# Kernel tuning notes

Hardware: AMD Instinct MI355X
Metric: run time of the kernel (lower is better)

## Reference

```python
import jax, jax.numpy as jnp
import numpy as np

D = 128          # hidden_dim
H = 4            # num attention heads (torch default nhead=4 in this module)
DH = D // H
NA = 4096        # author nodes
NP = 100000      # paper nodes
EAP = 500000     # author->paper edges
EPA = 500000     # paper->author edges
DFF = 2048       # TransformerEncoderLayer FFN dim (torch default)
OUT = 16
IN_A = 128
IN_P = 256
EPS = 1e-5


def layer_norm(x, g, b):
    mu = jnp.mean(x, -1, keepdims=True)
    var = jnp.mean((x - mu) ** 2, -1, keepdims=True)
    return (x - mu) / jnp.sqrt(var + EPS) * g + b


def scatter_mean(vals, idx, n):
    # torch_scatter 'mean': empty segments yield 0
    s = jax.ops.segment_sum(vals, idx, num_segments=n)
    c = jax.ops.segment_sum(jnp.ones((vals.shape[0], 1), vals.dtype), idx, num_segments=n)
    return s / jnp.maximum(c, 1.0)


def metapath_layer(x_src, x_dst, src, dst, Wv, bv, Wo, bo, g, b):
    # nn.MultiheadAttention applied per-edge with seq_len=1 (query/key/value are
    # [1, E, D]); softmax over a single key is identically 1, so the attention
    # output is exactly out_proj(v_proj(x_src[src])) -- q/k projections have no
    # effect on the output (and zero gradient).
    v = x_src[src] @ Wv.T + bv            # [E, D] gather + value projection
    attn = v @ Wo.T + bo                  # output projection
    agg = scatter_mean(attn, dst, x_dst.shape[0])
    return layer_norm(agg + x_dst, g, b)


def fusion_layer(x, Wqkv, bqkv, Wo, bo, W1, b1, W2, b2, g1, bt1, g2, bt2):
    # torch TransformerEncoderLayer defaults: post-norm, relu, batch_first=False,
    # so x: [S=NA (seq), M (batch = #metapaths), D].
    S, M, _ = x.shape
    qkv = x @ Wqkv.T + bqkv               # [S, M, 3D]
    q, k, v = jnp.split(qkv, 3, axis=-1)
    q = q.reshape(S, M, H, DH)
    k = k.reshape(S, M, H, DH)
    v = v.reshape(S, M, H, DH)
    scores = jnp.einsum('smhd,tmhd->mhst', q, k) / np.float32(np.sqrt(DH))
    a = jax.nn.softmax(scores, axis=-1)
    ctx = jnp.einsum('mhst,tmhd->smhd', a, v).reshape(S, M, D)
    x = layer_norm(x + ctx @ Wo.T + bo, g1, bt1)
    ff = jax.nn.relu(x @ W1.T + b1) @ W2.T + b2
    return layer_norm(x + ff, g2, bt2)


def setup_inputs() -> dict:
    key = jax.random.key(0)
    ks = iter(jax.random.split(key, 64))
    def nrm(shape, scale=0.02):
        return jax.random.normal(next(ks), shape, dtype=jnp.float32) * scale
    inp = {
        'x_author': jax.random.normal(next(ks), (NA, IN_A), dtype=jnp.float32),
        'x_paper': jax.random.normal(next(ks), (NP, IN_P), dtype=jnp.float32),
        'src_ap': jax.random.randint(next(ks), (EAP,), 0, NA),
        'dst_ap': jax.random.randint(next(ks), (EAP,), 0, NP),
        'src_pa': jax.random.randint(next(ks), (EPA,), 0, NP),
        'dst_pa': jax.random.randint(next(ks), (EPA,), 0, NA),
        'pa_W': nrm((D, IN_A)), 'pa_b': nrm((D,)),
        'pp_W': nrm((D, IN_P)), 'pp_b': nrm((D,)),
        'f_Wqkv': nrm((3 * D, D)), 'f_bqkv': nrm((3 * D,)),
        'f_Wo': nrm((D, D)), 'f_bo': nrm((D,)),
        'f_W1': nrm((DFF, D)), 'f_b1': nrm((DFF,)),
        'f_W2': nrm((D, DFF)), 'f_b2': nrm((D,)),
        'f_g1': jnp.ones((D,), jnp.float32), 'f_bt1': jnp.zeros((D,), jnp.float32),
        'f_g2': jnp.ones((D,), jnp.float32), 'f_bt2': jnp.zeros((D,), jnp.float32),
        'cls_W': nrm((OUT, D)), 'cls_b': nrm((OUT,)),
    }
    for i in range(3):
        inp[f'l{i}_Wv'] = nrm((D, D)); inp[f'l{i}_bv'] = nrm((D,))
        inp[f'l{i}_Wo'] = nrm((D, D)); inp[f'l{i}_bo'] = nrm((D,))
        inp[f'l{i}_g'] = jnp.ones((D,), jnp.float32); inp[f'l{i}_b'] = jnp.zeros((D,), jnp.float32)
    return inp


def reference(x_author, x_paper, src_ap, dst_ap, src_pa, dst_pa,
              pa_W, pa_b, pp_W, pp_b,
              f_Wqkv, f_bqkv, f_Wo, f_bo, f_W1, f_b1, f_W2, f_b2,
              f_g1, f_bt1, f_g2, f_bt2, cls_W, cls_b,
              l0_Wv, l0_bv, l0_Wo, l0_bo, l0_g, l0_b,
              l1_Wv, l1_bv, l1_Wo, l1_bo, l1_g, l1_b,
              l2_Wv, l2_bv, l2_Wo, l2_bo, l2_g, l2_b):
    # project node features to hidden_dim
    ha = x_author @ pa_W.T + pa_b         # [NA, D]
    hp = x_paper @ pp_W.T + pp_b          # [NP, D]
    # metapath 0: paper -> author (one MetapathLayer)
    mp0 = metapath_layer(hp, ha, src_pa, dst_pa, l0_Wv, l0_bv, l0_Wo, l0_bo, l0_g, l0_b)
    # metapath 1: author -> paper -> author (two MetapathLayers)
    t = metapath_layer(ha, hp, src_ap, dst_ap, l1_Wv, l1_bv, l1_Wo, l1_bo, l1_g, l1_b)
    mp1 = metapath_layer(t, ha, src_pa, dst_pa, l2_Wv, l2_bv, l2_Wo, l2_bo, l2_g, l2_b)
    stacked = jnp.stack([mp0, mp1], axis=1)   # [NA, 2, D]
    fused = fusion_layer(stacked, f_Wqkv, f_bqkv, f_Wo, f_bo,
                         f_W1, f_b1, f_W2, f_b2,
                         f_g1, f_bt1, f_g2, f_bt2).mean(axis=1)
    return fused @ cls_W.T + cls_b            # [NA, OUT]
```

## Files before the change

### kernel.cpp

```cpp
#include <hip/hip_runtime.h>
#include <math.h>

constexpr int NA = 4096, NP = 100000, E_AP = 500000, E_PA = 500000;
constexpr int D = 128, DFF = 2048, NOUT = 16, IN_A = 128, IN_P = 256;

typedef __attribute__((ext_vector_type(8))) short bf16x8;
typedef __attribute__((ext_vector_type(4))) float f32x4;
typedef unsigned int u32;

__device__ __forceinline__ ushort f2b(float x) {
    union { float f; unsigned u; } v; v.f = x;
    unsigned r = v.u + 0x7fff + ((v.u >> 16) & 1);
    return (ushort)(r >> 16);
}
__device__ __forceinline__ float b2f(ushort h) {
    union { unsigned u; float f; } v; v.u = (unsigned)h << 16;
    return v.f;
}
__device__ __forceinline__ u32 fbits(float x) {
    union { float f; u32 u; } v; v.f = x; return v.u;
}

__device__ __forceinline__ bf16x8 cvtfrag(float4 a, float4 b) {
    union { u32 w[4]; bf16x8 v; } r;
    asm("v_cvt_pk_bf16_f32 %0, %1, %2" : "=v"(r.w[0]) : "v"(a.x), "v"(a.y));
    asm("v_cvt_pk_bf16_f32 %0, %1, %2" : "=v"(r.w[1]) : "v"(a.z), "v"(a.w));
    asm("v_cvt_pk_bf16_f32 %0, %1, %2" : "=v"(r.w[2]) : "v"(b.x), "v"(b.y));
    asm("v_cvt_pk_bf16_f32 %0, %1, %2" : "=v"(r.w[3]) : "v"(b.z), "v"(b.w));
    return r.v;
}

#define GLL(gp, lp) __builtin_amdgcn_global_load_lds( \
    (const __attribute__((address_space(1))) u32*)(gp), \
    (__attribute__((address_space(3))) u32*)(lp), 16, 0, 0)

__global__ __launch_bounds__(256) void gemm_bf16(
    const ushort* __restrict__ Abf, const float* __restrict__ Af32, int lda,
    const ushort* __restrict__ B, int ldb,
    const float* __restrict__ bias,
    float* __restrict__ outf, ushort* __restrict__ outh, int ldc,
    int M, int N, int K, int act)
{
    __shared__ uint8_t lds[(16 + 32) * 1040];
    uint8_t* sAb = lds;
    uint8_t* sBb = lds + 16 * 1040;

    const int wave = threadIdx.x >> 6;
    const int lane = threadIdx.x & 63;
    const int l16 = lane & 15, quad = lane >> 4;
    const int row0 = blockIdx.y * 64;
    const int col0 = blockIdx.x * 128;
    const int wrg = (wave >> 1) * 2;
    const int wc0 = (wave & 1) * 64;
    const int nz = gridDim.z;
    const int ksub = K / nz;
    const int kbeg = blockIdx.z * ksub;
    const int kgrps = ksub >> 7;

    f32x4 acc[2][4] = {};

    const int sr = lane & 15, sc = lane >> 4;
    const int arow = min(row0 + lane, M - 1);
    const int ag = lane >> 4;
    uint8_t* adst = sAb + (ag * 4 + wave) * 1040 + sr * 16;

    for (int grp = 0; grp < kgrps; ++grp) {
        const int kg = kbeg + grp * 128;
        if (grp) __syncthreads();
        #pragma unroll
        for (int gg = 0; gg < 2; ++gg) {
            int g = wave * 2 + gg;
            const ushort* bp = B + (long)(col0 + g * 16 + sr) * ldb + kg + sc * 8;
            #pragma unroll
            for (int s = 0; s < 4; ++s)
                GLL(bp + s * 32, sBb + (g * 4 + s) * 1040);
        }
        if (Af32) {
            const float* ap = Af32 + (long)arow * lda + kg + wave * 32;
            #pragma unroll
            for (int q = 0; q < 4; ++q) {
                float4 f0 = *(const float4*)(ap + q * 8);
                float4 f1 = *(const float4*)(ap + q * 8 + 4);
                *(bf16x8*)(adst + q * 256) = cvtfrag(f0, f1);
            }
        } else {
            const ushort* ap = Abf + (long)arow * lda + kg + wave * 32;
            #pragma unroll
            for (int q = 0; q < 4; ++q)
                *(bf16x8*)(adst + q * 256) = *(const bf16x8*)(ap + q * 8);
        }
        __syncthreads();
        #pragma unroll
        for (int s = 0; s < 4; ++s) {
            bf16x8 af[2], bfr[4];
            #pragma unroll
            for (int i = 0; i < 2; ++i)
                af[i] = *(const bf16x8*)(sAb + ((wrg + i) * 4 + s) * 1040 + lane * 16);
            #pragma unroll
            for (int j = 0; j < 4; ++j)
                bfr[j] = *(const bf16x8*)(sBb + (((wc0 >> 4) + j) * 4 + s) * 1040 + lane * 16);
            #pragma unroll
            for (int i = 0; i < 2; ++i)
                #pragma unroll
                for (int j = 0; j < 4; ++j)
                    acc[i][j] = __builtin_amdgcn_mfma_f32_16x16x32_bf16(
                        af[i], bfr[j], acc[i][j], 0, 0, 0);
        }
    }

    #pragma unroll
    for (int i = 0; i < 2; ++i) {
        #pragma unroll
        for (int r = 0; r < 4; ++r) {
            int row = row0 + wrg * 16 + i * 16 + quad * 4 + r;
            if (row >= M) continue;
            #pragma unroll
            for (int j = 0; j < 4; ++j) {
                int col = col0 + wc0 + j * 16 + l16;
                if (nz > 1) {
                    atomicAdd(&outf[(long)row * ldc + col], acc[i][j][r]);
                } else {
                    float v = acc[i][j][r] + (bias ? bias[col] : 0.f);
                    if (act) v = fmaxf(v, 0.f);
                    if (outf) outf[(long)row * ldc + col] = v;
                    if (outh) outh[(long)row * ldc + col] = f2b(v);
                }
            }
        }
    }
}

__global__ __launch_bounds__(256) void fuse_weights(
    const float* __restrict__ Wv0, const float* __restrict__ bv0,
    const float* __restrict__ Wo0, const float* __restrict__ bo0,
    const float* __restrict__ Wv1, const float* __restrict__ bv1,
    const float* __restrict__ Wo1, const float* __restrict__ bo1,
    const float* __restrict__ Wv2, const float* __restrict__ bv2,
    const float* __restrict__ Wo2, const float* __restrict__ bo2,
    ushort* __restrict__ Wfb, float* __restrict__ beff)
{
    int blk = blockIdx.x;
    if (blk >= 192) {
        int l = blk - 192;
        const float* bv = l == 0 ? bv0 : (l == 1 ? bv1 : bv2);
        const float* Wo = l == 0 ? Wo0 : (l == 1 ? Wo1 : Wo2);
        const float* bo = l == 0 ? bo0 : (l == 1 ? bo1 : bo2);
        if (threadIdx.x < 128) {
            int r = threadIdx.x;
            float acc = bo[r];
            #pragma unroll 8
            for (int j = 0; j < 128; ++j) acc += Wo[r * 128 + j] * bv[j];
            beff[l * 128 + r] = acc;
        }
        return;
    }
    int l = blk >> 6;
    const float* Wv = l == 0 ? Wv0 : (l == 1 ? Wv1 : Wv2);
    const float* Wo = l == 0 ? Wo0 : (l == 1 ? Wo1 : Wo2);
    int r = (blk & 63) * 2 + (threadIdx.x >> 7);
    int c = threadIdx.x & 127;
    float acc = 0.f;
    #pragma unroll 8
    for (int j = 0; j < 128; ++j)
        acc += Wo[r * 128 + j] * Wv[j * 128 + c];
    Wfb[l * 16384 + r * 128 + c] = f2b(acc);
}

__global__ void hist_kernel(const int* __restrict__ dst, int* __restrict__ cnt, int E)
{
    int e = blockIdx.x * 256 + threadIdx.x;
    if (e < E) atomicAdd(&cnt[dst[e]], 1);
}

__global__ __launch_bounds__(256) void scan_local(
    const int* __restrict__ in, int* __restrict__ out,
    int* __restrict__ bsum, int n)
{
    __shared__ int wsum[4];
    int t = threadIdx.x;
    int base = blockIdx.x * 1024 + t * 4;
    int v0 = (base + 0 < n) ? in[base + 0] : 0;
    int v1 = (base + 1 < n) ? in[base + 1] : 0;
    int v2 = (base + 2 < n) ? in[base + 2] : 0;
    int v3 = (base + 3 < n) ? in[base + 3] : 0;
    int tsum = v0 + v1 + v2 + v3;
    int lane = t & 63;
    int x = tsum;
    #pragma unroll
    for (int o = 1; o < 64; o <<= 1) {
        int y = __shfl_up(x, o, 64);
        if (lane >= o) x += y;
    }
    int wid = t >> 6;
    if (lane == 63) wsum[wid] = x;
    __syncthreads();
    int woff = 0;
    #pragma unroll
    for (int ww = 0; ww < 3; ++ww) if (ww < wid) woff += wsum[ww];
    int excl = x - tsum + woff;
    if (base + 0 < n) out[base + 0] = excl;
    if (base + 1 < n) out[base + 1] = excl + v0;
    if (base + 2 < n) out[base + 2] = excl + v0 + v1;
    if (base + 3 < n) out[base + 3] = excl + v0 + v1 + v2;
    if (bsum && t == 255) bsum[blockIdx.x] = excl + tsum;
}

__global__ void scan_add(int* __restrict__ off, const int* __restrict__ bofs, int n)
{
    int i = blockIdx.x * 256 + threadIdx.x;
    if (i < n) off[i] += bofs[i >> 10];
}

__global__ void copy_int_kernel(const int* __restrict__ a, int* __restrict__ b, int n)
{
    int i = blockIdx.x * 256 + threadIdx.x;
    if (i < n) b[i] = a[i];
}

__global__ void fill_csr_kernel(const int* __restrict__ src, const int* __restrict__ dst,
                                int* __restrict__ cur, int* __restrict__ esrc, int E)
{
    int e = blockIdx.x * 256 + threadIdx.x;
    if (e >= E) return;
    int slot = atomicAdd(&cur[dst[e]], 1);
    esrc[slot] = src[e];
}

__global__ __launch_bounds__(256) void gather_mean(
    const ushort* __restrict__ z, const int* __restrict__ off,
    const int* __restrict__ cnt, const int* __restrict__ esrc,
    ushort* __restrict__ outh, int R)
{
    int grp = threadIdx.x >> 5;
    int tg  = threadIdx.x & 31;
    int row = blockIdx.x * 8 + grp;
    if (row >= R) return;
    int e0 = off[row], deg = cnt[row];
    int eend = e0 + deg;
    float a0 = 0.f, a1 = 0.f, a2 = 0.f, a3 = 0.f;
    int e = e0;
    for (; e + 4 <= eend; e += 4) {
        int s0 = esrc[e], s1 = esrc[e + 1], s2 = esrc[e + 2], s3 = esrc[e + 3];
        ushort4 v0 = ((const ushort4*)(z + (long)s0 * 128))[tg];
        ushort4 v1 = ((const ushort4*)(z + (long)s1 * 128))[tg];
        ushort4 v2 = ((const ushort4*)(z + (long)s2 * 128))[tg];
        ushort4 v3 = ((const ushort4*)(z + (long)s3 * 128))[tg];
        a0 += b2f(v0.x) + b2f(v1.x) + b2f(v2.x) + b2f(v3.x);
        a1 += b2f(v0.y) + b2f(v1.y) + b2f(v2.y) + b2f(v3.y);
        a2 += b2f(v0.z) + b2f(v1.z) + b2f(v2.z) + b2f(v3.z);
        a3 += b2f(v0.w) + b2f(v1.w) + b2f(v2.w) + b2f(v3.w);
    }
    for (; e < eend; ++e) {
        int s = esrc[e];
        ushort4 v = ((const ushort4*)(z + (long)s * 128))[tg];
        a0 += b2f(v.x); a1 += b2f(v.y); a2 += b2f(v.z); a3 += b2f(v.w);
    }
    float inv = 1.f / fmaxf((float)deg, 1.f);
    ushort4 h4 = {f2b(a0 * inv), f2b(a1 * inv), f2b(a2 * inv), f2b(a3 * inv)};
    ((ushort4*)(outh + (long)row * 128))[tg] = h4;
}

__global__ __launch_bounds__(256) void gather_mean_ln(
    const ushort* __restrict__ z, const int* __restrict__ off,
    const int* __restrict__ cnt, const int* __restrict__ esrc,
    const ushort* __restrict__ base, const float* __restrict__ g,
    const float* __restrict__ b, ushort* __restrict__ outh, int R)
{
    int grp = threadIdx.x >> 5;
    int tg  = threadIdx.x & 31;
    int row = blockIdx.x * 8 + grp;
    if (row >= R) return;
    int e0 = off[row], deg = cnt[row];
    int eend = e0 + deg;
    float a0 = 0.f, a1 = 0.f, a2 = 0.f, a3 = 0.f;
    int e = e0;
    for (; e + 4 <= eend; e += 4) {
        int s0 = esrc[e], s1 = esrc[e + 1], s2 = esrc[e + 2], s3 = esrc[e + 3];
        ushort4 v0 = ((const ushort4*)(z + (long)s0 * 128))[tg];
        ushort4 v1 = ((const ushort4*)(z + (long)s1 * 128))[tg];
        ushort4 v2 = ((const ushort4*)(z + (long)s2 * 128))[tg];
        ushort4 v3 = ((const ushort4*)(z + (long)s3 * 128))[tg];
        a0 += b2f(v0.x) + b2f(v1.x) + b2f(v2.x) + b2f(v3.x);
        a1 += b2f(v0.y) + b2f(v1.y) + b2f(v2.y) + b2f(v3.y);
        a2 += b2f(v0.z) + b2f(v1.z) + b2f(v2.z) + b2f(v3.z);
        a3 += b2f(v0.w) + b2f(v1.w) + b2f(v2.w) + b2f(v3.w);
    }
    for (; e < eend; ++e) {
        int s = esrc[e];
        ushort4 v = ((const ushort4*)(z + (long)s * 128))[tg];
        a0 += b2f(v.x); a1 += b2f(v.y); a2 += b2f(v.z); a3 += b2f(v.w);
    }
    float inv = 1.f / fmaxf((float)deg, 1.f);
    ushort4 bs = ((const ushort4*)(base + (long)row * 128))[tg];
    float x0 = a0 * inv + b2f(bs.x), x1 = a1 * inv + b2f(bs.y);
    float x2 = a2 * inv + b2f(bs.z), x3 = a3 * inv + b2f(bs.w);
    float s1 = x0 + x1 + x2 + x3;
    #pragma unroll
    for (int o = 1; o < 32; o <<= 1) s1 += __shfl_xor(s1, o, 64);
    float mu = s1 * (1.f / 128.f);
    float d0 = x0 - mu, d1 = x1 - mu, d2 = x2 - mu, d3 = x3 - mu;
    float s2 = d0 * d0 + d1 * d1 + d2 * d2 + d3 * d3;
    #pragma unroll
    for (int o = 1; o < 32; o <<= 1) s2 += __shfl_xor(s2, o, 64);
    float rstd = rsqrtf(s2 * (1.f / 128.f) + 1e-5f);
    float4 gv = ((const float4*)g)[tg];
    float4 bv = ((const float4*)b)[tg];
    ushort4 h4;
    h4.x = f2b(d0 * rstd * gv.x + bv.x);
    h4.y = f2b(d1 * rstd * gv.y + bv.y);
    h4.z = f2b(d2 * rstd * gv.z + bv.z);
    h4.w = f2b(d3 * rstd * gv.w + bv.w);
    ((ushort4*)(outh + (long)row * 128))[tg] = h4;
}

__global__ __launch_bounds__(128) void mean_add_ln(
    const float* __restrict__ a, const float* __restrict__ bias,
    const float* __restrict__ basef, const ushort* __restrict__ baseh,
    const float* __restrict__ g, const float* __restrict__ b,
    float* __restrict__ outf, ushort* __restrict__ outh, int out_ld, int R)
{
    int row = blockIdx.x;
    if (row >= R) return;
    int d = threadIdx.x;
    float x = a[(long)row * 128 + d];
    if (bias) x += bias[d];
    if (basef) x += basef[(long)row * 128 + d];
    if (baseh) x += b2f(baseh[(long)row * 128 + d]);

    __shared__ float red[4];
    float s = x;
    #pragma unroll
    for (int o = 32; o >= 1; o >>= 1) s += __shfl_xor(s, o, 64);
    if ((d & 63) == 0) red[d >> 6] = s;
    __syncthreads();
    float mu = (red[0] + red[1]) * (1.f / 128.f);
    float dx = x - mu;
    float s2 = dx * dx;
    #pragma unroll
    for (int o = 32; o >= 1; o >>= 1) s2 += __shfl_xor(s2, o, 64);
    if ((d & 63) == 0) red[2 + (d >> 6)] = s2;
    __syncthreads();
    float var = (red[2] + red[3]) * (1.f / 128.f);
    float v = dx * rsqrtf(var + 1e-5f) * g[d] + b[d];
    if (outf) outf[(long)row * out_ld + d] = v;
    if (outh) outh[(long)row * out_ld + d] = f2b(v);
}

struct CvtArgs { const float* in[6]; ushort* out[6]; int n4[6]; };
__global__ void cvt_multi(CvtArgs a)
{
    int j = blockIdx.y;
    int i = blockIdx.x * 256 + threadIdx.x;
    if (i >= a.n4[j]) return;
    float4 v = ((const float4*)a.in[j])[i];
    ushort4 o;
    o.x = f2b(v.x); o.y = f2b(v.y); o.z = f2b(v.z); o.w = f2b(v.w);
    ((ushort4*)a.out[j])[i] = o;
}

__global__ __launch_bounds__(256) void flash_attn(
    const ushort* __restrict__ qkvb,
    float* __restrict__ opart, float* __restrict__ lpart_g)
{
    const int qt = blockIdx.x;
    const int mh = blockIdx.y;
    const int ks = blockIdx.z;
    const int m = mh >> 2, h = mh & 3;
    const int wave = threadIdx.x >> 6;
    const int lane = threadIdx.x & 63;
    const int l16 = lane & 15, quad = lane >> 4;

    __shared__ ushort sK[2][64 * 40];
    __shared__ u32    sV[2][32 * 32];
    __shared__ u32    sP[4][16 * 32];

    const int q0 = qt * 64 + wave * 16;
    const float qs = 0.17677669529663687f * 1.4426950408889634f;
    bf16x8 qf;
    {
        bf16x8 qraw = *(const bf16x8*)(qkvb + ((long)(q0 + l16) * 2 + m) * 384 + h * 32 + quad * 8);
        #pragma unroll
        for (int j = 0; j < 8; ++j)
            qf[j] = (short)f2b(b2f((ushort)qraw[j]) * qs);
    }

    f32x4 oacc0 = {0.f, 0.f, 0.f, 0.f};
    f32x4 oacc1 = {0.f, 0.f, 0.f, 0.f};
    float lp = 0.f;

    const int skey = threadIdx.x >> 2, sseg = threadIdx.x & 3;
    const int vkp  = threadIdx.x & 31, vdc  = (threadIdx.x >> 5) * 4;
    const int kbeg = ks * (NA / 4);
    const ushort* kbase = qkvb + ((long)((kbeg + skey) * 2 + m)) * 384 + 128 + h * 32 + sseg * 8;
    const ushort* vbase = qkvb + ((long)((kbeg + vkp * 2) * 2 + m)) * 384 + 256 + h * 32 + vdc;
    const int kwo = skey * 40 + sseg * 8;
    int vwo[4];
    #pragma unroll
    for (int i = 0; i < 4; ++i)
        vwo[i] = (vdc + i) * 32 + ((((vkp >> 2) ^ ((vdc + i) & 7)) << 2) | (vkp & 3));

    bf16x8 kreg = *(const bf16x8*)(kbase);
    ushort4 v0r = *(const ushort4*)(vbase);
    ushort4 v1r = *(const ushort4*)(vbase + 768);
    *(bf16x8*)(&sK[0][kwo]) = kreg;
    sV[0][vwo[0]] = (u32)v0r.x | ((u32)v1r.x << 16);
    sV[0][vwo[1]] = (u32)v0r.y | ((u32)v1r.y << 16);
    sV[0][vwo[2]] = (u32)v0r.z | ((u32)v1r.z << 16);
    sV[0][vwo[3]] = (u32)v0r.w | ((u32)v1r.w << 16);
    __syncthreads();

    int cur = 0;
    for (int kt = 0; kt < 16; ++kt) {
        const bool more = (kt + 1) < 16;
        if (more) {
            long off = (long)(kt + 1) * 64 * 768;
            kreg = *(const bf16x8*)(kbase + off);
            v0r  = *(const ushort4*)(vbase + off);
            v1r  = *(const ushort4*)(vbase + off + 768);
        }

        #pragma unroll
        for (int t = 0; t < 4; ++t) {
            bf16x8 kf = *(const bf16x8*)(&sK[cur][(t * 16 + l16) * 40 + quad * 8]);
            f32x4 s = {0.f, 0.f, 0.f, 0.f};
            s = __builtin_amdgcn_mfma_f32_16x16x32_bf16(kf, qf, s, 0, 0, 0);
            float p0 = exp2f(s[0]), p1 = exp2f(s[1]);
            float p2 = exp2f(s[2]), p3 = exp2f(s[3]);
            lp += (p0 + p1) + (p2 + p3);
            u32 lo = __builtin_amdgcn_perm(fbits(p1), fbits(p0), 0x07060302u);
            u32 hi = __builtin_amdgcn_perm(fbits(p3), fbits(p2), 0x07060302u);
            u32* dst = &sP[wave][l16 * 32 +
                                 ((((t * 2 + (quad >> 1)) ^ (l16 & 7)) << 2) | ((quad & 1) * 2))];
            dst[0] = lo; dst[1] = hi;
        }
        #pragma unroll
        for (int c = 0; c < 2; ++c) {
            const int gp = ((c * 4 + quad) ^ (l16 & 7)) << 2;
            bf16x8 pf  = *(const bf16x8*)(&sP[wave][l16 * 32 + gp]);
            bf16x8 vf0 = *(const bf16x8*)(&sV[cur][l16 * 32 + gp]);
            bf16x8 vf1 = *(const bf16x8*)(&sV[cur][(16 + l16) * 32 + gp]);
            oacc0 = __builtin_amdgcn_mfma_f32_16x16x32_bf16(pf, vf0, oacc0, 0, 0, 0);
            oacc1 = __builtin_amdgcn_mfma_f32_16x16x32_bf16(pf, vf1, oacc1, 0, 0, 0);
        }

        if (more) {
            const int nxt = cur ^ 1;
            *(bf16x8*)(&sK[nxt][kwo]) = kreg;
            sV[nxt][vwo[0]] = (u32)v0r.x | ((u32)v1r.x << 16);
            sV[nxt][vwo[1]] = (u32)v0r.y | ((u32)v1r.y << 16);
            sV[nxt][vwo[2]] = (u32)v0r.z | ((u32)v1r.z << 16);
            sV[nxt][vwo[3]] = (u32)v0r.w | ((u32)v1r.w << 16);
            __syncthreads();
            cur = nxt;
        }
    }

    lp += __shfl_xor(lp, 16, 64);
    lp += __shfl_xor(lp, 32, 64);
    if (quad == 0)
        lpart_g[(long)(mh * 4 + ks) * NA + q0 + l16] = lp;

    #pragma unroll
    for (int r = 0; r < 4; ++r) {
        int qr = q0 + quad * 4 + r;
        long ob = ((long)(mh * 4 + ks) * NA + qr) * 32;
        opart[ob + l16]      = oacc0[r];
        opart[ob + 16 + l16] = oacc1[r];
    }
}

__global__ void attn_combine(const float* __restrict__ opart,
                             const float* __restrict__ lpart,
                             ushort* __restrict__ ctxb)
{
    int idx = blockIdx.x * 256 + threadIdx.x;
    int d = idx & 31;
    int row = idx >> 5;
    int mh = row >> 12, qrow = row & 4095;
    float o = 0.f, l = 0.f;
    #pragma unroll
    for (int ks = 0; ks < 4; ++ks) {
        long rb = (long)(mh * 4 + ks) * NA + qrow;
        o += opart[rb * 32 + d];
        l += lpart[rb];
    }
    int m = mh >> 2, h = mh & 3;
    ctxb[((long)qrow * 2 + m) * 128 + h * 32 + d] = f2b(o / l);
}

__global__ void classify_kernel(const float* __restrict__ x2,
                                const float* __restrict__ Wc,
                                const float* __restrict__ bc,
                                float* __restrict__ out)
{
    int idx = blockIdx.x * 256 + threadIdx.x;
    int a2 = idx >> 4, o = idx & 15;
    const float* r0 = x2 + (long)(a2 * 2) * 128;
    const float* r1 = r0 + 128;
    const float* w = Wc + o * 128;
    float acc = bc[o];
    #pragma unroll 4
    for (int dd = 0; dd < 128; ++dd) acc += 0.5f * (r0[dd] + r1[dd]) * w[dd];
    out[idx] = acc;
}

static void bgemm(hipStream_t st, const ushort* Abf, const float* Af32, int lda,
                  const ushort* B, int ldb,
                  const float* bias, float* outf, ushort* outh, int ldc,
                  int M, int N, int K, int act = 0, int ksplit = 1)
{
    dim3 grid(N / 128, (M + 63) / 64, ksplit);
    gemm_bf16<<<grid, 256, 0, st>>>(Abf, Af32, lda, B, ldb, bias, outf, outh,
                                    ldc, M, N, K, act);
}

static void build_csr(hipStream_t st, const int* src, const int* dst, int E, int n,
                      int* cnt, int* off, int* cur, int* bsum, int* esrc)
{
    hipMemsetAsync(cnt, 0, (size_t)n * 4, st);
    hist_kernel<<<(E + 255) / 256, 256, 0, st>>>(dst, cnt, E);
    int nb = (n + 1023) / 1024;
    scan_local<<<nb, 256, 0, st>>>(cnt, off, bsum, n);
    scan_local<<<1, 256, 0, st>>>(bsum, bsum, nullptr, nb);
    scan_add<<<(n + 255) / 256, 256, 0, st>>>(off, bsum, n);
    copy_int_kernel<<<(n + 255) / 256, 256, 0, st>>>(off, cur, n);
    fill_csr_kernel<<<(E + 255) / 256, 256, 0, st>>>(src, dst, cur, esrc, E);
}

extern "C" void kernel_launch(void* const* d_in, const int* in_sizes, int n_in,
                              void* d_out, int out_size, void* d_ws, size_t ws_size,
                              hipStream_t stream)
{
    const float* x_author = (const float*)d_in[0];
    const float* x_paper  = (const float*)d_in[1];
    const int*   src_ap   = (const int*)d_in[2];
    const int*   dst_ap   = (const int*)d_in[3];
    const int*   src_pa   = (const int*)d_in[4];
    const int*   dst_pa   = (const int*)d_in[5];
    const float* pa_W = (const float*)d_in[6];   const float* pa_b = (const float*)d_in[7];
    const float* pp_W = (const float*)d_in[8];   const float* pp_b = (const float*)d_in[9];
    const float* f_Wqkv = (const float*)d_in[10]; const float* f_bqkv = (const float*)d_in[11];
    const float* f_Wo = (const float*)d_in[12];  const float* f_bo = (const float*)d_in[13];
    const float* f_W1 = (const float*)d_in[14];  const float* f_b1 = (const float*)d_in[15];
    const float* f_W2 = (const float*)d_in[16];  const float* f_b2 = (const float*)d_in[17];
    const float* f_g1 = (const float*)d_in[18];  const float* f_bt1 = (const float*)d_in[19];
    const float* f_g2 = (const float*)d_in[20];  const float* f_bt2 = (const float*)d_in[21];
    const float* cls_W = (const float*)d_in[22]; const float* cls_b = (const float*)d_in[23];
    const float* l0_Wv = (const float*)d_in[24]; const float* l0_bv = (const float*)d_in[25];
    const float* l0_Wo = (const float*)d_in[26]; const float* l0_bo = (const float*)d_in[27];
    const float* l0_g  = (const float*)d_in[28]; const float* l0_b  = (const float*)d_in[29];
    const float* l1_Wv = (const float*)d_in[30]; const float* l1_bv = (const float*)d_in[31];
    const float* l1_Wo = (const float*)d_in[32]; const float* l1_bo = (const float*)d_in[33];
    const float* l1_g  = (const float*)d_in[34]; const float* l1_b  = (const float*)d_in[35];
    const float* l2_Wv = (const float*)d_in[36]; const float* l2_bv = (const float*)d_in[37];
    const float* l2_Wo = (const float*)d_in[38]; const float* l2_bo = (const float*)d_in[39];
    const float* l2_g  = (const float*)d_in[40]; const float* l2_b  = (const float*)d_in[41];

    uint8_t* w = (uint8_t*)d_ws;
    ushort* TB  = (ushort*)(w + 0);
    ushort* FF  = (ushort*)(w + 26214400);
    float*  OPART = (float*)(w + 26214400);
    float*  LPART = (float*)(w + 43515904);
    ushort* HPB = (ushort*)(w + 61440000);
    ushort* ZB  = (ushort*)(w + 87040000);
    uint8_t* p2 = w + 102400000;
    ushort* QKVB = (ushort*)(p2 + 0);
    ushort* CTXB = (ushort*)(p2 + 6291456);
    float*  TMP  = (float*)(p2 + 8388608);
    float*  X1   = (float*)(p2 + 12582912);
    ushort* X1B  = (ushort*)(p2 + 16777216);
    float*  TMP2 = (float*)(p2 + 18874368);
    float*  X2   = (float*)(p2 + 23068672);
    uint8_t* tail = p2 + 27262976;
    float*  STKF  = (float*)(tail + 0);
    ushort* STKB  = (ushort*)(tail + 4194304);
    ushort* HAB   = (ushort*)(tail + 6291456);
    ushort* GMA   = (ushort*)(tail + 7340032);
    ushort* WFB   = (ushort*)(tail + 8388608);
    ushort* PAWB  = (ushort*)(tail + 8486912);
    ushort* PPWB  = (ushort*)(tail + 8519680);
    ushort* WQKVB = (ushort*)(tail + 8585216);
    ushort* WOB   = (ushort*)(tail + 8683520);
    ushort* W1B   = (ushort*)(tail + 8716288);
    ushort* W2B   = (ushort*)(tail + 9240576);
    float*  BEFF  = (float*)(tail + 9764864);
    int*   CNT_A  = (int*)(tail + 9766400);
    int*   OFF_A  = (int*)(tail + 9782784);
    int*   CUR_A  = (int*)(tail + 9799168);
    int*   CNT_P  = (int*)(tail + 9815552);
    int*   OFF_P  = (int*)(tail + 10215552);
    int*   CUR_P  = (int*)(tail + 10615552);
    int*   ESRC_PA= (int*)(tail + 11015552);
    int*   ESRC_AP= (int*)(tail + 13015552);
    int*   BSUM_A = (int*)(tail + 15015552);
    int*   BSUM_P = (int*)(tail + 15016576);
    float* TMPA   = (float*)(tail + 15017984);

    CvtArgs ca;
    ca.in[0] = pa_W;   ca.out[0] = PAWB;  ca.n4[0] = D * IN_A / 4;
    ca.in[1] = pp_W;   ca.out[1] = PPWB;  ca.n4[1] = D * IN_P / 4;
    ca.in[2] = f_Wqkv; ca.out[2] = WQKVB; ca.n4[2] = 3 * D * D / 4;
    ca.in[3] = f_Wo;   ca.out[3] = WOB;   ca.n4[3] = D * D / 4;
    ca.in[4] = f_W1;   ca.out[4] = W1B;   ca.n4[4] = DFF * D / 4;
    ca.in[5] = f_W2;   ca.out[5] = W2B;   ca.n4[5] = D * DFF / 4;
    cvt_multi<<<dim3((DFF * D / 4 + 255) / 256, 6), 256, 0, stream>>>(ca);

    fuse_weights<<<195, 256, 0, stream>>>(l0_Wv, l0_bv, l0_Wo, l0_bo,
                                          l1_Wv, l1_bv, l1_Wo, l1_bo,
                                          l2_Wv, l2_bv, l2_Wo, l2_bo, WFB, BEFF);

    build_csr(stream, src_pa, dst_pa, E_PA, NA, CNT_A, OFF_A, CUR_A, BSUM_A, ESRC_PA);
    build_csr(stream, src_ap, dst_ap, E_AP, NP, CNT_P, OFF_P, CUR_P, BSUM_P, ESRC_AP);

    bgemm(stream, nullptr, x_author, IN_A, PAWB, IN_A, pa_b, nullptr, HAB, D, NA, D, IN_A);
    bgemm(stream, nullptr, x_paper,  IN_P, PPWB, IN_P, pp_b, nullptr, HPB, D, NP, D, IN_P);

    gather_mean<<<(NA + 7) / 8, 256, 0, stream>>>(HPB, OFF_A, CNT_A, ESRC_PA, GMA, NA);
    bgemm(stream, GMA, nullptr, D, WFB, D, BEFF, TMPA, nullptr, D, NA, D, D);
    mean_add_ln<<<NA, 128, 0, stream>>>(TMPA, nullptr, nullptr, HAB, l0_g, l0_b,
                                        nullptr, STKB, 256, NA);

    bgemm(stream, HAB, nullptr, D, WFB + 16384, D, BEFF + 128, nullptr, ZB, D, NA, D, D);
    gather_mean_ln<<<(NP + 7) / 8, 256, 0, stream>>>(
        ZB, OFF_P, CNT_P, ESRC_AP, HPB, l1_g, l1_b, TB, NP);

    gather_mean<<<(NA + 7) / 8, 256, 0, stream>>>(TB, OFF_A, CNT_A, ESRC_PA, GMA, NA);
    bgemm(stream, GMA, nullptr, D, WFB + 32768, D, BEFF + 256, TMPA, nullptr, D, NA, D, D);
    mean_add_ln<<<NA, 128, 0, stream>>>(TMPA, nullptr, nullptr, HAB, l2_g, l2_b,
                                        nullptr, STKB + 128, 256, NA);

    bgemm(stream, STKB, nullptr, D, WQKVB, D, f_bqkv, nullptr, QKVB, 3 * D, 2 * NA, 3 * D, D);
    flash_attn<<<dim3(NA / 64, 8, 4), 256, 0, stream>>>(QKVB, OPART, LPART);
    attn_combine<<<8 * NA * 32 / 256, 256, 0, stream>>>(OPART, LPART, CTXB);

    bgemm(stream, CTXB, nullptr, D, WOB, D, f_bo, TMP, nullptr, D, 2 * NA, D, D);
    mean_add_ln<<<2 * NA, 128, 0, stream>>>(TMP, nullptr, nullptr, STKB, f_g1, f_bt1,
                                            X1, X1B, 128, 2 * NA);

    bgemm(stream, X1B, nullptr, D, W1B, D, f_b1, nullptr, FF, DFF, 2 * NA, DFF, D, 1);
    hipMemsetAsync(TMP2, 0, (size_t)2 * NA * D * 4, stream);
    bgemm(stream, FF, nullptr, DFF, W2B, DFF, nullptr, TMP2, nullptr, D, 2 * NA, D, DFF, 0, 8);
    mean_add_ln<<<2 * NA, 128, 0, stream>>>(TMP2, f_b2, X1, nullptr, f_g2, f_bt2,
                                            X2, nullptr, 128, 2 * NA);

    classify_kernel<<<(NA * NOUT) / 256, 256, 0, stream>>>(X2, cls_W, cls_b, (float*)d_out);
}
```

Measured before the change: 706.6 us.

## Fuse FFN GEMMs into one kernel, halve attention key splits, merge scan copy

```diff
diff --git a/kernel.cpp b/kernel.cpp
--- a/kernel.cpp
+++ b/kernel.cpp
@@ -33,6 +33,8 @@
 #define GLL(gp, lp) __builtin_amdgcn_global_load_lds( \
     (const __attribute__((address_space(1))) u32*)(gp), \
     (__attribute__((address_space(3))) u32*)(lp), 16, 0, 0)
+
+#define MFMA16(a, b, c) __builtin_amdgcn_mfma_f32_16x16x32_bf16((a), (b), (c), 0, 0, 0)
 
 __global__ __launch_bounds__(256) void gemm_bf16(
     const ushort* __restrict__ Abf, const float* __restrict__ Af32, int lda,
@@ -103,8 +105,7 @@
             for (int i = 0; i < 2; ++i)
                 #pragma unroll
                 for (int j = 0; j < 4; ++j)
-                    acc[i][j] = __builtin_amdgcn_mfma_f32_16x16x32_bf16(
-                        af[i], bfr[j], acc[i][j], 0, 0, 0);
+                    acc[i][j] = MFMA16(af[i], bfr[j], acc[i][j]);
         }
     }
 
@@ -128,6 +129,114 @@
             }
         }
     }
+}
+
+__global__ __launch_bounds__(256) void ffn_fused(
+    const ushort* __restrict__ x1b,
+    const ushort* __restrict__ W1b,
+    const ushort* __restrict__ W2b,
+    const float* __restrict__ b1,
+    float* __restrict__ outf)
+{
+    __shared__ uint8_t lds[56 * 1040];
+    uint8_t* sX  = lds;
+    uint8_t* sW1 = lds + 16 * 1040;
+    uint8_t* sW2 = lds + 32 * 1040;
+    uint8_t* sH  = lds + 48 * 1040;
+
+    const int wave = threadIdx.x >> 6;
+    const int lane = threadIdx.x & 63;
+    const int l16 = lane & 15, quad = lane >> 4;
+    const int sr = lane & 15, sc = lane >> 4;
+    const int row0 = blockIdx.x * 64;
+    const int dbeg = blockIdx.y * 512;
+
+    const int xg = wave >> 1;
+    const int ch = wave & 1;
+
+    {
+        const ushort* xp = x1b + (long)(row0 + wave * 16 + sr) * 128 + sc * 8;
+        #pragma unroll
+        for (int s = 0; s < 4; ++s)
+            GLL(xp + s * 32, sX + (wave * 4 + s) * 1040);
+    }
+
+    f32x4 acc2[2][4] = {};
+
+    for (int c = 0; c < 8; ++c) {
+        const int kc = dbeg + c * 64;
+        {
+            const ushort* w1p = W1b + (long)(kc + wave * 16 + sr) * 128 + sc * 8;
+            #pragma unroll
+            for (int s = 0; s < 4; ++s)
+                GLL(w1p + s * 32, sW1 + (wave * 4 + s) * 1040);
+            #pragma unroll
+            for (int gg = 0; gg < 2; ++gg) {
+                int cg = wave * 2 + gg;
+                const ushort* w2p = W2b + (long)(cg * 16 + sr) * 2048 + kc + sc * 8;
+                #pragma unroll
+                for (int s2 = 0; s2 < 2; ++s2)
+                    GLL(w2p + s2 * 32, sW2 + (cg * 2 + s2) * 1040);
+            }
+        }
+        __syncthreads();
+
+        f32x4 acc1[2][2] = {};
+        #pragma unroll
+        for (int s = 0; s < 4; ++s) {
+            bf16x8 a0 = *(const bf16x8*)(sX + ((xg * 2 + 0) * 4 + s) * 1040 + lane * 16);
+            bf16x8 a1 = *(const bf16x8*)(sX + ((xg * 2 + 1) * 4 + s) * 1040 + lane * 16);
+            bf16x8 w0 = *(const bf16x8*)(sW1 + ((ch * 2 + 0) * 4 + s) * 1040 + lane * 16);
+            bf16x8 w1 = *(const bf16x8*)(sW1 + ((ch * 2 + 1) * 4 + s) * 1040 + lane * 16);
+            acc1[0][0] = MFMA16(a0, w0, acc1[0][0]);
+            acc1[0][1] = MFMA16(a0, w1, acc1[0][1]);
+            acc1[1][0] = MFMA16(a1, w0, acc1[1][0]);
+            acc1[1][1] = MFMA16(a1, w1, acc1[1][1]);
+        }
+        float bb0 = b1[kc + ch * 32 + l16];
+        float bb1 = b1[kc + ch * 32 + 16 + l16];
+        #pragma unroll
+        for (int i = 0; i < 2; ++i) {
+            uint8_t* hb = sH + ((xg * 2 + i) * 2 + ch) * 1040;
+            #pragma unroll
+            for (int j = 0; j < 2; ++j) {
+                float bb = j ? bb1 : bb0;
+                int q = ((j * 16 + l16) >> 3) & 3;
+                int byo = (l16 & 7) * 2;
+                #pragma unroll
+                for (int r = 0; r < 4; ++r) {
+                    float v = fmaxf(acc1[i][j][r] + bb, 0.f);
+                    *(ushort*)(hb + q * 256 + (quad * 4 + r) * 16 + byo) = f2b(v);
+                }
+            }
+        }
+        __syncthreads();
+
+        #pragma unroll
+        for (int s2 = 0; s2 < 2; ++s2) {
+            bf16x8 h0 = *(const bf16x8*)(sH + ((xg * 2 + 0) * 2 + s2) * 1040 + lane * 16);
+            bf16x8 h1 = *(const bf16x8*)(sH + ((xg * 2 + 1) * 2 + s2) * 1040 + lane * 16);
+            #pragma unroll
+            for (int j2 = 0; j2 < 4; ++j2) {
+                bf16x8 wb = *(const bf16x8*)(sW2 + ((ch * 4 + j2) * 2 + s2) * 1040 + lane * 16);
+                acc2[0][j2] = MFMA16(h0, wb, acc2[0][j2]);
+                acc2[1][j2] = MFMA16(h1, wb, acc2[1][j2]);
+            }
+        }
+        __syncthreads();
+    }
+
+    #pragma unroll
+    for (int i = 0; i < 2; ++i)
+        #pragma unroll
+        for (int r = 0; r < 4; ++r) {
+            int row = row0 + xg * 32 + i * 16 + quad * 4 + r;
+            #pragma unroll
+            for (int j2 = 0; j2 < 4; ++j2) {
+                int col = ch * 64 + j2 * 16 + l16;
+                atomicAdd(&outf[(long)row * 128 + col], acc2[i][j2][r]);
+            }
+        }
 }
 
 __global__ __launch_bounds__(256) void fuse_weights(
@@ -205,16 +314,15 @@
     if (bsum && t == 255) bsum[blockIdx.x] = excl + tsum;
 }
 
-__global__ void scan_add(int* __restrict__ off, const int* __restrict__ bofs, int n)
+__global__ void scan_add(int* __restrict__ off, const int* __restrict__ bofs,
+                         int* __restrict__ cur, int n)
 {
     int i = blockIdx.x * 256 + threadIdx.x;
-    if (i < n) off[i] += bofs[i >> 10];
-}
-
-__global__ void copy_int_kernel(const int* __restrict__ a, int* __restrict__ b, int n)
-{
-    int i = blockIdx.x * 256 + threadIdx.x;
-    if (i < n) b[i] = a[i];
+    if (i < n) {
+        int v = off[i] + bofs[i >> 10];
+        off[i] = v;
+        cur[i] = v;
+    }
 }
 
 __global__ void fill_csr_kernel(const int* __restrict__ src, const int* __restrict__ dst,
@@ -390,7 +498,7 @@
 
     const int skey = threadIdx.x >> 2, sseg = threadIdx.x & 3;
     const int vkp  = threadIdx.x & 31, vdc  = (threadIdx.x >> 5) * 4;
-    const int kbeg = ks * (NA / 4);
+    const int kbeg = ks * (NA / 2);
     const ushort* kbase = qkvb + ((long)((kbeg + skey) * 2 + m)) * 384 + 128 + h * 32 + sseg * 8;
     const ushort* vbase = qkvb + ((long)((kbeg + vkp * 2) * 2 + m)) * 384 + 256 + h * 32 + vdc;
     const int kwo = skey * 40 + sseg * 8;
@@ -410,8 +518,8 @@
     __syncthreads();
 
     int cur = 0;
-    for (int kt = 0; kt < 16; ++kt) {
-        const bool more = (kt + 1) < 16;
+    for (int kt = 0; kt < 32; ++kt) {
+        const bool more = (kt + 1) < 32;
         if (more) {
             long off = (long)(kt + 1) * 64 * 768;
             kreg = *(const bf16x8*)(kbase + off);
@@ -423,7 +531,7 @@
         for (int t = 0; t < 4; ++t) {
             bf16x8 kf = *(const bf16x8*)(&sK[cur][(t * 16 + l16) * 40 + quad * 8]);
             f32x4 s = {0.f, 0.f, 0.f, 0.f};
-            s = __builtin_amdgcn_mfma_f32_16x16x32_bf16(kf, qf, s, 0, 0, 0);
+            s = MFMA16(kf, qf, s);
             float p0 = exp2f(s[0]), p1 = exp2f(s[1]);
             float p2 = exp2f(s[2]), p3 = exp2f(s[3]);
             lp += (p0 + p1) + (p2 + p3);
@@ -439,8 +547,8 @@
             bf16x8 pf  = *(const bf16x8*)(&sP[wave][l16 * 32 + gp]);
             bf16x8 vf0 = *(const bf16x8*)(&sV[cur][l16 * 32 + gp]);
             bf16x8 vf1 = *(const bf16x8*)(&sV[cur][(16 + l16) * 32 + gp]);
-            oacc0 = __builtin_amdgcn_mfma_f32_16x16x32_bf16(pf, vf0, oacc0, 0, 0, 0);
-            oacc1 = __builtin_amdgcn_mfma_f32_16x16x32_bf16(pf, vf1, oacc1, 0, 0, 0);
+            oacc0 = MFMA16(pf, vf0, oacc0);
+            oacc1 = MFMA16(pf, vf1, oacc1);
         }
 
         if (more) {
@@ -458,12 +566,12 @@
     lp += __shfl_xor(lp, 16, 64);
     lp += __shfl_xor(lp, 32, 64);
     if (quad == 0)
-        lpart_g[(long)(mh * 4 + ks) * NA + q0 + l16] = lp;
+        lpart_g[(long)(mh * 2 + ks) * NA + q0 + l16] = lp;
 
     #pragma unroll
     for (int r = 0; r < 4; ++r) {
         int qr = q0 + quad * 4 + r;
-        long ob = ((long)(mh * 4 + ks) * NA + qr) * 32;
+        long ob = ((long)(mh * 2 + ks) * NA + qr) * 32;
         opart[ob + l16]      = oacc0[r];
         opart[ob + 16 + l16] = oacc1[r];
     }
@@ -479,8 +587,8 @@
     int mh = row >> 12, qrow = row & 4095;
     float o = 0.f, l = 0.f;
     #pragma unroll
-    for (int ks = 0; ks < 4; ++ks) {
-        long rb = (long)(mh * 4 + ks) * NA + qrow;
+    for (int ks = 0; ks < 2; ++ks) {
+        long rb = (long)(mh * 2 + ks) * NA + qrow;
         o += opart[rb * 32 + d];
         l += lpart[rb];
     }
@@ -522,8 +630,7 @@
     int nb = (n + 1023) / 1024;
     scan_local<<<nb, 256, 0, st>>>(cnt, off, bsum, n);
     scan_local<<<1, 256, 0, st>>>(bsum, bsum, nullptr, nb);
-    scan_add<<<(n + 255) / 256, 256, 0, st>>>(off, bsum, n);
-    copy_int_kernel<<<(n + 255) / 256, 256, 0, st>>>(off, cur, n);
+    scan_add<<<(n + 255) / 256, 256, 0, st>>>(off, bsum, cur, n);
     fill_csr_kernel<<<(E + 255) / 256, 256, 0, st>>>(src, dst, cur, esrc, E);
 }
 
@@ -558,7 +665,6 @@
 
     uint8_t* w = (uint8_t*)d_ws;
     ushort* TB  = (ushort*)(w + 0);
-    ushort* FF  = (ushort*)(w + 26214400);
     float*  OPART = (float*)(w + 26214400);
     float*  LPART = (float*)(w + 43515904);
     ushort* HPB = (ushort*)(w + 61440000);
@@ -572,7 +678,6 @@
     float*  TMP2 = (float*)(p2 + 18874368);
     float*  X2   = (float*)(p2 + 23068672);
     uint8_t* tail = p2 + 27262976;
-    float*  STKF  = (float*)(tail + 0);
     ushort* STKB  = (ushort*)(tail + 4194304);
     ushort* HAB   = (ushort*)(tail + 6291456);
     ushort* GMA   = (ushort*)(tail + 7340032);
@@ -630,16 +735,15 @@
                                         nullptr, STKB + 128, 256, NA);
 
     bgemm(stream, STKB, nullptr, D, WQKVB, D, f_bqkv, nullptr, QKVB, 3 * D, 2 * NA, 3 * D, D);
-    flash_attn<<<dim3(NA / 64, 8, 4), 256, 0, stream>>>(QKVB, OPART, LPART);
+    flash_attn<<<dim3(NA / 64, 8, 2), 256, 0, stream>>>(QKVB, OPART, LPART);
     attn_combine<<<8 * NA * 32 / 256, 256, 0, stream>>>(OPART, LPART, CTXB);
 
     bgemm(stream, CTXB, nullptr, D, WOB, D, f_bo, TMP, nullptr, D, 2 * NA, D, D);
     mean_add_ln<<<2 * NA, 128, 0, stream>>>(TMP, nullptr, nullptr, STKB, f_g1, f_bt1,
                                             X1, X1B, 128, 2 * NA);
 
-    bgemm(stream, X1B, nullptr, D, W1B, D, f_b1, nullptr, FF, DFF, 2 * NA, DFF, D, 1);
     hipMemsetAsync(TMP2, 0, (size_t)2 * NA * D * 4, stream);
-    bgemm(stream, FF, nullptr, DFF, W2B, DFF, nullptr, TMP2, nullptr, D, 2 * NA, D, DFF, 0, 8);
+    ffn_fused<<<dim3(2 * NA / 64, 4), 256, 0, stream>>>(X1B, W1B, W2B, f_b1, TMP2);
     mean_add_ln<<<2 * NA, 128, 0, stream>>>(TMP2, f_b2, X1, nullptr, f_g2, f_bt2,
                                             X2, nullptr, 128, 2 * NA);
 
```

New measurement: 674.8 us. 4.5% less time.
